# Performance work log

Measured on AMD Instinct MI355X. Metric: run time of the kernel, lower is better.

The kernel has to match this reference:

```python
import jax, jax.numpy as jnp
import numpy as np

B, T, D = 4, 256, 1024
E, DL, TOPK, H = 16, 64, 2, 4


def setup_inputs() -> dict:
    key = jax.random.key(0)
    ks = jax.random.split(key, 12)
    n = lambda k, s: (0.02 * jax.random.normal(k, s)).astype(jnp.float32)
    return dict(
        x=jax.random.normal(ks[0], (B, T, D), dtype=jnp.float32),
        w_down=n(ks[1], (E * DL, D)),
        pos_embed=n(ks[2], (1, E, DL)),
        gp_w=n(ks[3], (DL, D)), gp_b=jnp.zeros((DL,), jnp.float32),
        attn_in_w=n(ks[4], (3 * DL, DL)), attn_in_b=jnp.zeros((3 * DL,), jnp.float32),
        attn_out_w=n(ks[5], (DL, DL)), attn_out_b=jnp.zeros((DL,), jnp.float32),
        ln_w=jnp.ones((DL,), jnp.float32), ln_b=jnp.zeros((DL,), jnp.float32),
        ls_w=n(ks[6], (1, DL)), ls_b=jnp.zeros((1,), jnp.float32),
        g1_w=n(ks[7], (2 * DL, DL)), g1_b=jnp.zeros((2 * DL,), jnp.float32),
        g2_w=n(ks[8], (E, 2 * DL)), g2_b=jnp.zeros((E,), jnp.float32),
        w_up=n(ks[9], (E, DL, D)),
    )


def reference(x, w_down, pos_embed, gp_w, gp_b, attn_in_w, attn_in_b,
              attn_out_w, attn_out_b, ln_w, ln_b, ls_w, ls_b,
              g1_w, g1_b, g2_w, g2_b, w_up):
    Bq, Tq, Dm = x.shape
    N = Bq * Tq
    xf = x.reshape(N, Dm)
    # per-token per-expert low-rank features [N, E, DL]
    ef = (xf @ w_down.T).reshape(N, E, DL)
    # global context per batch element -> [B, DL]
    gctx = x.mean(axis=1) @ gp_w.T + gp_b
    gtok = jnp.repeat(gctx, Tq, axis=0)[:, None, :]  # [N, 1, DL]
    seq = jnp.concatenate([gtok, ef + pos_embed], axis=1)  # [N, E+1, DL]
    # tiny multihead self-attention over E+1 tokens, eval mode (no dropout)
    qkv = seq @ attn_in_w.T + attn_in_b
    q, k, v = jnp.split(qkv, 3, axis=-1)
    hd = DL // H
    sh = lambda t: t.reshape(N, E + 1, H, hd).transpose(0, 2, 1, 3)
    q, k, v = sh(q), sh(k), sh(v)
    scores = jnp.einsum('nhqd,nhkd->nhqk', q, k) / np.float32(np.sqrt(hd))
    attn = jax.nn.softmax(scores, axis=-1)
    ctx = jnp.einsum('nhqk,nhkd->nhqd', attn, v).transpose(0, 2, 1, 3).reshape(N, E + 1, DL)
    attn_out = ctx @ attn_out_w.T + attn_out_b
    h = attn_out + seq
    mu = h.mean(-1, keepdims=True)
    var = h.var(-1, keepdims=True)
    hn = (h - mu) / jnp.sqrt(var + 1e-5) * ln_w + ln_b
    refined = hn[:, 1:, :]  # drop global token -> [N, E, DL]
    local_logits = (refined @ ls_w.T + ls_b)[..., 0]  # [N, E]
    gb = jax.nn.gelu(gctx @ g1_w.T + g1_b, approximate=False) @ g2_w.T + g2_b  # [B, E]
    logits = local_logits + jnp.repeat(gb, Tq, axis=0)
    probs = jax.nn.softmax(logits, axis=-1)
    tw, ti = jax.lax.top_k(probs, TOPK)
    tw = tw / tw.sum(-1, keepdims=True)
    sel = jnp.take_along_axis(ef, ti[..., None], axis=1)  # [N, K, DL]
    act = jax.nn.gelu(sel, approximate=False)
    # gather per-token expert up-projections and batched vec-mat
    eo = jnp.einsum('nkd,nkdm->nkm', act, w_up[ti])  # [N, K, D]
    out = (eo * tw[..., None]).sum(axis=1).reshape(Bq, Tq, Dm)
    mean_prob = probs.mean(axis=0)
    one_hot = jnp.zeros_like(probs).at[jnp.arange(N)[:, None], ti].set(1.0)
    aux_loss = E * jnp.sum(mean_prob * one_hot.mean(axis=0))
    return out, aux_loss
```

## Files before the change

### kernel.cpp

```cpp
#include <hip/hip_runtime.h>
#include <math.h>

#define NB 4
#define TT 256
#define DMODEL 1024
#define NE 16
#define DLQ 64
#define NH 4
#define HD 16
#define SEQL 17
#define NTOK 1024

static constexpr size_t WS_EF    = 0;
static constexpr size_t WS_AH    = 1048576;
static constexpr size_t WS_AL    = 1572864;
static constexpr size_t WS_BH    = 2097152;
static constexpr size_t WS_BL    = 2621440;
static constexpr size_t WS_P1    = 3145728;
static constexpr size_t WS_ACT   = 4194304;
static constexpr size_t WS_AIWFH = 4259840;
static constexpr size_t WS_AIWFL = 4265984;
static constexpr size_t WS_AOWFH = 4272128;
static constexpr size_t WS_AOWFL = 4274176;
static constexpr size_t WS_PR    = 4308992;
static constexpr size_t WS_TI    = 4325376;
static constexpr size_t WS_GCTX  = 4326400;
static constexpr size_t WS_GB    = 4326656;

typedef __attribute__((ext_vector_type(8))) short short8;
typedef __attribute__((ext_vector_type(4))) float f32x4;

__device__ __forceinline__ float gelu_exact(float x) {
    return 0.5f * x * (1.0f + erff(x * 0.70710678118654752f));
}

__device__ __forceinline__ unsigned short f2bf(float f) {
    unsigned int u = __float_as_uint(f);
    unsigned int r = (u + 0x7fffu + ((u >> 16) & 1u)) >> 16;
    return (unsigned short)r;
}
__device__ __forceinline__ float bf2f(unsigned short h) {
    return __uint_as_float(((unsigned int)h) << 16);
}

#define DPP_ADD(v, ctrl) { int _m = __builtin_amdgcn_update_dpp(0, __float_as_int(v), ctrl, 0xF, 0xF, true); \
                           v += __int_as_float(_m); }
__device__ __forceinline__ float rsum16(float v) {
    DPP_ADD(v, 0x128);
    DPP_ADD(v, 0x124);
    DPP_ADD(v, 0x122);
    DPP_ADD(v, 0x121);
    return v;
}
__device__ __forceinline__ float rsum64(float v) {
    v = rsum16(v);
    v += __shfl_xor(v, 16);
    v += __shfl_xor(v, 32);
    return v;
}

__global__ __launch_bounds__(256) void k_prep(const float* __restrict__ x,
                                              const float* __restrict__ wdn,
                                              const float* __restrict__ aiw,
                                              const float* __restrict__ aow,
                                              const float* __restrict__ gp_w,
                                              const float* __restrict__ gp_b,
                                              const float* __restrict__ g1_w,
                                              const float* __restrict__ g1_b,
                                              const float* __restrict__ g2_w,
                                              const float* __restrict__ g2_b,
                                              float* __restrict__ ws) {
    __shared__ float xm[DMODEL];
    __shared__ float gc[DLQ];
    __shared__ float gb1[128];
    int bi = blockIdx.x;
    int tid = threadIdx.x;
    if (bi < 1024) {
        int which = bi >> 9;
        int t = (bi & 511) * 256 + tid;
        int row = t >> 7;
        int col0 = (t & 127) * 8;
        const float* src = which ? wdn : x;
        unsigned short* hp = (unsigned short*)(ws + (which ? WS_BH : WS_AH));
        unsigned short* lp = (unsigned short*)(ws + (which ? WS_BL : WS_AL));
        float4 v0 = *(const float4*)(src + (size_t)row * DMODEL + col0);
        float4 v1 = *(const float4*)(src + (size_t)row * DMODEL + col0 + 4);
        float vv[8] = {v0.x, v0.y, v0.z, v0.w, v1.x, v1.y, v1.z, v1.w};
        unsigned short h8[8], l8[8];
#pragma unroll
        for (int j = 0; j < 8; ++j) {
            h8[j] = f2bf(vv[j]);
            l8[j] = f2bf(vv[j] - bf2f(h8[j]));
        }
        int nb = row >> 6, kb = col0 >> 6;
        int st = (row & 63) >> 4;
        int ks = (col0 & 63) >> 5;
        int ln = (row & 15) + (((col0 >> 3) & 3) << 4);
        size_t off = (size_t)(nb * 16 + kb) * 4096 + st * 1024 + ks * 512 + ln * 8;
        *(short8*)(hp + off) = *(short8*)h8;
        *(short8*)(lp + off) = *(short8*)l8;
    } else if (bi < 1028) {
        int b = bi - 1024;
        int wv = tid >> 6, l = tid & 63;
        {
            const float* xb = x + (size_t)b * TT * DMODEL + tid * 4;
            float4 a = {0.f, 0.f, 0.f, 0.f};
#pragma unroll 4
            for (int t2 = 0; t2 < TT; ++t2) {
                float4 v = *(const float4*)(xb + (size_t)t2 * DMODEL);
                a.x += v.x; a.y += v.y; a.z += v.z; a.w += v.w;
            }
            const float inv_t = 1.0f / (float)TT;
            xm[tid * 4 + 0] = a.x * inv_t;
            xm[tid * 4 + 1] = a.y * inv_t;
            xm[tid * 4 + 2] = a.z * inv_t;
            xm[tid * 4 + 3] = a.w * inv_t;
        }
        __syncthreads();
        {
            const float* xp = xm + l * 16;
            float4 xv0 = *(const float4*)(xp);
            float4 xv1 = *(const float4*)(xp + 4);
            float4 xv2 = *(const float4*)(xp + 8);
            float4 xv3 = *(const float4*)(xp + 12);
            for (int rq = 0; rq < 4; ++rq) {
                int o = wv * 16 + rq * 4;
                float s[4];
#pragma unroll
                for (int r = 0; r < 4; ++r) {
                    const float* wr = gp_w + (size_t)(o + r) * DMODEL + l * 16;
                    float4 w0 = *(const float4*)(wr);
                    float4 w1 = *(const float4*)(wr + 4);
                    float4 w2 = *(const float4*)(wr + 8);
                    float4 w3 = *(const float4*)(wr + 12);
                    s[r] = w0.x * xv0.x + w0.y * xv0.y + w0.z * xv0.z + w0.w * xv0.w +
                           w1.x * xv1.x + w1.y * xv1.y + w1.z * xv1.z + w1.w * xv1.w +
                           w2.x * xv2.x + w2.y * xv2.y + w2.z * xv2.z + w2.w * xv2.w +
                           w3.x * xv3.x + w3.y * xv3.y + w3.z * xv3.z + w3.w * xv3.w;
                }
#pragma unroll
                for (int r = 0; r < 4; ++r) s[r] = rsum64(s[r]);
                if (l == 0) {
#pragma unroll
                    for (int r = 0; r < 4; ++r) {
                        float v = s[r] + gp_b[o + r];
                        gc[o + r] = v;
                        ws[WS_GCTX + b * DLQ + o + r] = v;
                    }
                }
            }
        }
        __syncthreads();
        {
            float gcl = gc[l];
            for (int rq = 0; rq < 8; ++rq) {
                int o = wv * 32 + rq * 4;
                float s[4];
#pragma unroll
                for (int r = 0; r < 4; ++r) s[r] = gcl * g1_w[(size_t)(o + r) * DLQ + l];
#pragma unroll
                for (int r = 0; r < 4; ++r) s[r] = rsum64(s[r]);
                if (l == 0) {
#pragma unroll
                    for (int r = 0; r < 4; ++r) gb1[o + r] = gelu_exact(s[r] + g1_b[o + r]);
                }
            }
        }
        __syncthreads();
        {
            float v0 = gb1[l * 2], v1 = gb1[l * 2 + 1];
            int o = wv * 4;
            float s[4];
#pragma unroll
            for (int r = 0; r < 4; ++r)
                s[r] = v0 * g2_w[(size_t)(o + r) * 128 + l * 2] +
                       v1 * g2_w[(size_t)(o + r) * 128 + l * 2 + 1];
#pragma unroll
            for (int r = 0; r < 4; ++r) s[r] = rsum64(s[r]);
            if (l == 0) {
#pragma unroll
                for (int r = 0; r < 4; ++r) ws[WS_GB + b * NE + o + r] = s[r] + g2_b[o + r];
            }
        }
    } else {
        unsigned short* fh = (unsigned short*)(ws + WS_AIWFH);
        unsigned short* fl = (unsigned short*)(ws + WS_AIWFL);
        for (int idx = tid; idx < 12 * 2 * 64; idx += 256) {
            int nt = idx >> 7, kf = (idx >> 6) & 1, l = idx & 63;
            int row = nt * 16 + (l & 15);
            int k = kf * 32 + ((l >> 4) << 3);
            const float* src = aiw + (size_t)row * DLQ + k;
            unsigned short h8[8], l8[8];
#pragma unroll
            for (int j = 0; j < 8; ++j) {
                h8[j] = f2bf(src[j]);
                l8[j] = f2bf(src[j] - bf2f(h8[j]));
            }
            size_t off = (size_t)(nt * 2 + kf) * 512 + l * 8;
            *(short8*)(fh + off) = *(short8*)h8;
            *(short8*)(fl + off) = *(short8*)l8;
        }
        unsigned short* gh = (unsigned short*)(ws + WS_AOWFH);
        unsigned short* gl = (unsigned short*)(ws + WS_AOWFL);
        for (int idx = tid; idx < 4 * 2 * 64; idx += 256) {
            int nt = idx >> 7, kf = (idx >> 6) & 1, l = idx & 63;
            int row = nt * 16 + (l & 15);
            int k = kf * 32 + ((l >> 4) << 3);
            const float* src = aow + (size_t)row * DLQ + k;
            unsigned short h8[8], l8[8];
#pragma unroll
            for (int j = 0; j < 8; ++j) {
                h8[j] = f2bf(src[j]);
                l8[j] = f2bf(src[j] - bf2f(h8[j]));
            }
            size_t off = (size_t)(nt * 2 + kf) * 512 + l * 8;
            *(short8*)(gh + off) = *(short8*)h8;
            *(short8*)(gl + off) = *(short8*)l8;
        }
    }
}

__global__ __launch_bounds__(256) void k_ef_mfma(float* __restrict__ ws) {
    __shared__ __attribute__((aligned(16))) unsigned short smem[16384];
    int tid = threadIdx.x;
    int bi = blockIdx.x;

    int xcd = bi & 7;
    int g   = bi >> 3;
    int kz  = g >> 5;
    int rem = g & 31;
    int nb  = (xcd >> 1) * 4 + (rem >> 3);
    int mb  = (xcd & 1) * 8 + (rem & 7);

    const unsigned short* AhP = (const unsigned short*)(ws + WS_AH);
    const unsigned short* AlP = (const unsigned short*)(ws + WS_AL);
    const unsigned short* BhP = (const unsigned short*)(ws + WS_BH);
    const unsigned short* BlP = (const unsigned short*)(ws + WS_BL);
    int w = tid >> 6, l = tid & 63;
    int wn = (w >> 1) * 32, wm = (w & 1) * 32;
    int stA = wn >> 4, stB = wm >> 4;
    f32x4 acc00 = {0.f, 0.f, 0.f, 0.f}, acc01 = acc00, acc10 = acc00, acc11 = acc00;

    for (int it = 0; it < 8; ++it) {
        int kb = kz * 8 + it;
        const char* srcs[4] = {
            (const char*)(AhP + (size_t)(nb * 16 + kb) * 4096),
            (const char*)(AlP + (size_t)(nb * 16 + kb) * 4096),
            (const char*)(BhP + (size_t)(mb * 16 + kb) * 4096),
            (const char*)(BlP + (size_t)(mb * 16 + kb) * 4096)};
#pragma unroll
        for (int p = 0; p < 4; ++p) {
#pragma unroll
            for (int h = 0; h < 2; ++h) {
                __builtin_amdgcn_global_load_lds(
                    (const __attribute__((address_space(1))) void*)(srcs[p] + h * 4096 + tid * 16),
                    (__attribute__((address_space(3))) void*)((char*)smem + p * 8192 + h * 4096 + tid * 16),
                    16, 0, 0);
            }
        }
        __syncthreads();
        const unsigned short* Ah = smem;
        const unsigned short* Al = smem + 4096;
        const unsigned short* Bh = smem + 8192;
        const unsigned short* Bl = smem + 12288;
#pragma unroll
        for (int ks = 0; ks < 2; ++ks) {
            short8 ah0 = *(const short8*)(Ah + (stA + 0) * 1024 + ks * 512 + l * 8);
            short8 ah1 = *(const short8*)(Ah + (stA + 1) * 1024 + ks * 512 + l * 8);
            short8 al0 = *(const short8*)(Al + (stA + 0) * 1024 + ks * 512 + l * 8);
            short8 al1 = *(const short8*)(Al + (stA + 1) * 1024 + ks * 512 + l * 8);
            short8 bh0 = *(const short8*)(Bh + (stB + 0) * 1024 + ks * 512 + l * 8);
            short8 bh1 = *(const short8*)(Bh + (stB + 1) * 1024 + ks * 512 + l * 8);
            short8 bl0 = *(const short8*)(Bl + (stB + 0) * 1024 + ks * 512 + l * 8);
            short8 bl1 = *(const short8*)(Bl + (stB + 1) * 1024 + ks * 512 + l * 8);
            acc00 = __builtin_amdgcn_mfma_f32_16x16x32_bf16(ah0, bh0, acc00, 0, 0, 0);
            acc00 = __builtin_amdgcn_mfma_f32_16x16x32_bf16(al0, bh0, acc00, 0, 0, 0);
            acc00 = __builtin_amdgcn_mfma_f32_16x16x32_bf16(ah0, bl0, acc00, 0, 0, 0);
            acc01 = __builtin_amdgcn_mfma_f32_16x16x32_bf16(ah0, bh1, acc01, 0, 0, 0);
            acc01 = __builtin_amdgcn_mfma_f32_16x16x32_bf16(al0, bh1, acc01, 0, 0, 0);
            acc01 = __builtin_amdgcn_mfma_f32_16x16x32_bf16(ah0, bl1, acc01, 0, 0, 0);
            acc10 = __builtin_amdgcn_mfma_f32_16x16x32_bf16(ah1, bh0, acc10, 0, 0, 0);
            acc10 = __builtin_amdgcn_mfma_f32_16x16x32_bf16(al1, bh0, acc10, 0, 0, 0);
            acc10 = __builtin_amdgcn_mfma_f32_16x16x32_bf16(ah1, bl0, acc10, 0, 0, 0);
            acc11 = __builtin_amdgcn_mfma_f32_16x16x32_bf16(ah1, bh1, acc11, 0, 0, 0);
            acc11 = __builtin_amdgcn_mfma_f32_16x16x32_bf16(al1, bh1, acc11, 0, 0, 0);
            acc11 = __builtin_amdgcn_mfma_f32_16x16x32_bf16(ah1, bl1, acc11, 0, 0, 0);
        }
        __syncthreads();
    }
    int cr = (l >> 4) * 4, cc = l & 15;
    int n0 = nb * 64, m0 = mb * 64;
    float* P = ws + (kz == 0 ? WS_EF : WS_P1);
#pragma unroll
    for (int r = 0; r < 4; ++r) {
        P[(size_t)(n0 + wn + cr + r) * DMODEL + (m0 + wm + cc)]           = acc00[r];
        P[(size_t)(n0 + wn + cr + r) * DMODEL + (m0 + wm + 16 + cc)]      = acc01[r];
        P[(size_t)(n0 + wn + 16 + cr + r) * DMODEL + (m0 + wm + cc)]      = acc10[r];
        P[(size_t)(n0 + wn + 16 + cr + r) * DMODEL + (m0 + wm + 16 + cc)] = acc11[r];
    }
}

__global__ __launch_bounds__(128) void k_attn2(const float* __restrict__ pos_embed,
                                               const float* __restrict__ attn_in_b,
                                               const float* __restrict__ attn_out_b,
                                               const float* __restrict__ ln_w,
                                               const float* __restrict__ ln_b,
                                               const float* __restrict__ ls_w,
                                               const float* __restrict__ ls_b,
                                               float* __restrict__ ws) {
    int n = blockIdx.x;
    int w = threadIdx.x >> 6;
    int l = threadIdx.x & 63;
    int b = n >> 8;

    __shared__ float qkv[SEQL * 200];
    __shared__ __attribute__((aligned(16))) char ubuf[8192];
    __shared__ __attribute__((aligned(16))) unsigned short ctxH[1024];
    __shared__ __attribute__((aligned(16))) unsigned short ctxL[1024];
    __shared__ float lgv_sh[NE];
    unsigned short* sH = (unsigned short*)ubuf;
    unsigned short* sL = (unsigned short*)(ubuf + 4096);
    float* ao = (float*)ubuf;

    float seqc[SEQL];
    {
        const float* efp0 = ws + WS_EF + (size_t)n * DMODEL;
        const float* efp1 = ws + WS_P1 + (size_t)n * DMODEL;
        float gcv = ws[WS_GCTX + b * DLQ + l];
#pragma unroll
        for (int i = 0; i < SEQL; ++i) {
            float s = (i == 0) ? gcv
                               : efp0[(i - 1) * DLQ + l] + efp1[(i - 1) * DLQ + l] +
                                 pos_embed[(i - 1) * DLQ + l];
            seqc[i] = s;
            int lo_r = w * 9, hi_r = w * 9 + 8;
            if (i >= lo_r && i <= hi_r && i < SEQL) {
                unsigned short hs = f2bf(s);
                unsigned short lsv = f2bf(s - bf2f(hs));
                int mt = i >> 4;
                int ls = (i & 15) + (((l >> 3) & 3) << 4);
                int kf = l >> 5;
                int j = l & 7;
                size_t off = (size_t)(mt * 2 + kf) * 512 + ls * 8 + j;
                sH[off] = hs;
                sL[off] = lsv;
            }
        }
    }
    __syncthreads();

    {
        const unsigned short* fh = (const unsigned short*)(ws + WS_AIWFH);
        const unsigned short* fl = (const unsigned short*)(ws + WS_AIWFL);
        f32x4 acc[6][2];
#pragma unroll
        for (int t = 0; t < 6; ++t)
#pragma unroll
            for (int m = 0; m < 2; ++m) acc[t][m] = (f32x4){0.f, 0.f, 0.f, 0.f};
#pragma unroll
        for (int kf = 0; kf < 2; ++kf) {
            short8 ah0 = *(const short8*)(sH + (0 * 2 + kf) * 512 + l * 8);
            short8 ah1 = *(const short8*)(sH + (1 * 2 + kf) * 512 + l * 8);
            short8 al0 = *(const short8*)(sL + (0 * 2 + kf) * 512 + l * 8);
            short8 al1 = *(const short8*)(sL + (1 * 2 + kf) * 512 + l * 8);
#pragma unroll
            for (int t = 0; t < 6; ++t) {
                int nt = w * 6 + t;
                short8 bh = *(const short8*)(fh + (size_t)(nt * 2 + kf) * 512 + l * 8);
                short8 bl = *(const short8*)(fl + (size_t)(nt * 2 + kf) * 512 + l * 8);
                acc[t][0] = __builtin_amdgcn_mfma_f32_16x16x32_bf16(ah0, bh, acc[t][0], 0, 0, 0);
                acc[t][0] = __builtin_amdgcn_mfma_f32_16x16x32_bf16(al0, bh, acc[t][0], 0, 0, 0);
                acc[t][0] = __builtin_amdgcn_mfma_f32_16x16x32_bf16(ah0, bl, acc[t][0], 0, 0, 0);
                acc[t][1] = __builtin_amdgcn_mfma_f32_16x16x32_bf16(ah1, bh, acc[t][1], 0, 0, 0);
                acc[t][1] = __builtin_amdgcn_mfma_f32_16x16x32_bf16(al1, bh, acc[t][1], 0, 0, 0);
                acc[t][1] = __builtin_amdgcn_mfma_f32_16x16x32_bf16(ah1, bl, acc[t][1], 0, 0, 0);
            }
        }
#pragma unroll
        for (int t = 0; t < 6; ++t) {
            int col = (w * 6 + t) * 16 + (l & 15);
            float bias = attn_in_b[col];
#pragma unroll
            for (int r = 0; r < 4; ++r) {
                int row = (l >> 4) * 4 + r;
                qkv[row * 200 + col] = acc[t][0][r] + bias;
            }
            if ((l >> 4) == 0) qkv[16 * 200 + col] = acc[t][1][0] + bias;
        }
    }
    __syncthreads();

    {
        int g = l >> 4;
        float kc[SEQL], vc[SEQL];
#pragma unroll
        for (int j = 0; j < SEQL; ++j) {
            kc[j] = qkv[j * 200 + 64 + g * 16 + (l & 15)];
            vc[j] = qkv[j * 200 + 128 + l];
        }
        for (int i = w * 8 + 1; i <= w * 8 + 8; ++i) {
            float qi = qkv[i * 200 + g * 16 + (l & 15)];
            float sj[SEQL];
#pragma unroll
            for (int j = 0; j < SEQL; ++j) {
                sj[j] = rsum16(qi * kc[j]) * 0.25f;
            }
            float m = sj[0];
#pragma unroll
            for (int j = 1; j < SEQL; ++j) m = fmaxf(m, sj[j]);
            float ssum = 0.f;
#pragma unroll
            for (int j = 0; j < SEQL; ++j) { sj[j] = __expf(sj[j] - m); ssum += sj[j]; }
            float inv = 1.f / ssum;
            float c = 0.f;
#pragma unroll
            for (int j = 0; j < SEQL; ++j) c += sj[j] * vc[j];
            c *= inv;
            unsigned short ch = f2bf(c);
            unsigned short cl = f2bf(c - bf2f(ch));
            int ls = ((i - 1) & 15) + (((l >> 3) & 3) << 4);
            int kf = l >> 5;
            int j2 = l & 7;
            size_t off = (size_t)kf * 512 + ls * 8 + j2;
            ctxH[off] = ch;
            ctxL[off] = cl;
        }
    }
    __syncthreads();

    {
        const unsigned short* gh = (const unsigned short*)(ws + WS_AOWFH);
        const unsigned short* gl = (const unsigned short*)(ws + WS_AOWFL);
        f32x4 acc[2];
        acc[0] = (f32x4){0.f, 0.f, 0.f, 0.f};
        acc[1] = acc[0];
#pragma unroll
        for (int kf = 0; kf < 2; ++kf) {
            short8 ah = *(const short8*)(ctxH + kf * 512 + l * 8);
            short8 al = *(const short8*)(ctxL + kf * 512 + l * 8);
#pragma unroll
            for (int t = 0; t < 2; ++t) {
                int nt = w * 2 + t;
                short8 bh = *(const short8*)(gh + (size_t)(nt * 2 + kf) * 512 + l * 8);
                short8 bl = *(const short8*)(gl + (size_t)(nt * 2 + kf) * 512 + l * 8);
                acc[t] = __builtin_amdgcn_mfma_f32_16x16x32_bf16(ah, bh, acc[t], 0, 0, 0);
                acc[t] = __builtin_amdgcn_mfma_f32_16x16x32_bf16(al, bh, acc[t], 0, 0, 0);
                acc[t] = __builtin_amdgcn_mfma_f32_16x16x32_bf16(ah, bl, acc[t], 0, 0, 0);
            }
        }
        __syncthreads();
#pragma unroll
        for (int t = 0; t < 2; ++t) {
            int col = (w * 2 + t) * 16 + (l & 15);
            float bias = attn_out_b[col];
#pragma unroll
            for (int r = 0; r < 4; ++r) {
                int row = (l >> 4) * 4 + r;
                ao[row * 72 + col] = acc[t][r] + bias;
            }
        }
    }
    __syncthreads();

    float rs[SEQL];
#pragma unroll
    for (int i = 1; i < SEQL; ++i) rs[i] = seqc[i] + ao[(i - 1) * 72 + l];

    float c1 = ln_w[l] * ls_w[l];
    float c1sum = rsum64(c1);
    float c0sum = rsum64(ln_b[l] * ls_w[l]);
    float lsb0 = ls_b[0];
#pragma unroll
    for (int ee = 0; ee < 8; ++ee) {
        int e = w * 8 + ee;
        float x = rs[e + 1];
        float s1 = rsum64(x);
        float s2 = rsum64(x * x);
        float s3 = rsum64(x * c1);
        float mu = s1 * (1.0f / DLQ);
        float var = s2 * (1.0f / DLQ) - mu * mu;
        float rstd = rsqrtf(var + 1e-5f);
        float lgv = rstd * (s3 - mu * c1sum) + c0sum + lsb0 + ws[WS_GB + b * NE + e];
        if (l == 0) lgv_sh[e] = lgv;
    }
    __syncthreads();

    if (w == 0) {
        float p[NE];
        float lgv[NE];
#pragma unroll
        for (int e = 0; e < NE; ++e) lgv[e] = lgv_sh[e];
        float m = lgv[0];
#pragma unroll
        for (int e = 1; e < NE; ++e) m = fmaxf(m, lgv[e]);
        float ssum = 0.f;
#pragma unroll
        for (int e = 0; e < NE; ++e) { p[e] = __expf(lgv[e] - m); ssum += p[e]; }
        float inv = 1.f / ssum;
#pragma unroll
        for (int e = 0; e < NE; ++e) p[e] *= inv;
        int t0 = 0; float b0 = p[0];
#pragma unroll
        for (int e = 1; e < NE; ++e) if (p[e] > b0) { b0 = p[e]; t0 = e; }
        int t1 = -1; float b1 = -1.f;
#pragma unroll
        for (int e = 0; e < NE; ++e) if (e != t0 && p[e] > b1) { b1 = p[e]; t1 = e; }

        float sw = b0 + b1;
        float tw0 = b0 / sw, tw1 = b1 / sw;
        unsigned short* actp = (unsigned short*)(ws + WS_ACT);
        float efv0 = ws[WS_EF + (size_t)n * DMODEL + t0 * DLQ + l] +
                     ws[WS_P1 + (size_t)n * DMODEL + t0 * DLQ + l];
        float efv1 = ws[WS_EF + (size_t)n * DMODEL + t1 * DLQ + l] +
                     ws[WS_P1 + (size_t)n * DMODEL + t1 * DLQ + l];
        actp[(size_t)(n * 2 + 0) * 64 + l] = f2bf(gelu_exact(efv0) * tw0);
        actp[(size_t)(n * 2 + 1) * 64 + l] = f2bf(gelu_exact(efv1) * tw1);
        if (l == 0) {
#pragma unroll
            for (int e = 0; e < NE; ++e) ws[WS_PR + (size_t)n * NE + e] = p[e];
            ((int*)(ws + WS_TI))[n] = t0 | (t1 << 8);
        }
    }
}

__global__ __launch_bounds__(256) void k_moe_gemm(const float* __restrict__ w_up,
                                                  float* __restrict__ ws,
                                                  float* __restrict__ out) {
    __shared__ int lst[2048];
    __shared__ int lcnt;
    __shared__ float wsum[4][NE];
    __shared__ int hist[NE];
    int tid = threadIdx.x;
    int wv = tid >> 6, l = tid & 63;

    if (blockIdx.x == NE) {
        if (blockIdx.y != 0) return;
        if (tid < NE) hist[tid] = 0;
        __syncthreads();
        {
            const int* tip = (const int*)(ws + WS_TI);
#pragma unroll
            for (int c = 0; c < 4; ++c) {
                int pk = tip[tid * 4 + c];
                atomicAdd(&hist[pk & 0xff], 1);
                atomicAdd(&hist[(pk >> 8) & 0xff], 1);
            }
        }
        float p[NE];
#pragma unroll
        for (int e = 0; e < NE; ++e) p[e] = 0.f;
        const float* pr = ws + WS_PR + (size_t)tid * 64;
#pragma unroll
        for (int r = 0; r < 4; ++r)
#pragma unroll
            for (int q = 0; q < 4; ++q) {
                float4 v = *(const float4*)(pr + r * 16 + q * 4);
                p[q * 4 + 0] += v.x; p[q * 4 + 1] += v.y;
                p[q * 4 + 2] += v.z; p[q * 4 + 3] += v.w;
            }
#pragma unroll
        for (int e = 0; e < NE; ++e) p[e] = rsum64(p[e]);
        if (l == 0) {
#pragma unroll
            for (int e = 0; e < NE; ++e) wsum[wv][e] = p[e];
        }
        __syncthreads();
        if (tid == 0) {
            float s = 0.f;
#pragma unroll
            for (int e = 0; e < NE; ++e) {
                float sp = wsum[0][e] + wsum[1][e] + wsum[2][e] + wsum[3][e];
                s += sp * (float)hist[e];
            }
            out[(size_t)NTOK * DMODEL] = (float)NE * s / ((float)NTOK * (float)NTOK);
        }
        return;
    }

    int e = blockIdx.x, ct = blockIdx.y;
    if (tid == 0) lcnt = 0;
    __syncthreads();
    {
        const int* tip = (const int*)(ws + WS_TI);
#pragma unroll
        for (int c = 0; c < 4; ++c) {
            int tok = wv * 256 + c * 64 + l;
            int pk = tip[tok];
            bool m1 = ((pk >> 8) & 0xff) == e;
            bool m = ((pk & 0xff) == e) || m1;
            unsigned long long mask = __ballot(m);
            int base = 0;
            if (l == 0 && mask) base = atomicAdd(&lcnt, __popcll(mask));
            base = __shfl(base, 0);
            if (m) {
                int pos = base + __popcll(mask & ((1ull << l) - 1ull));
                lst[pos] = tok * 2 + (m1 ? 1 : 0);
            }
        }
    }
    __syncthreads();
    int cnt = lcnt;
    if (cnt == 0) return;

    int col = ct * 64 + wv * 16 + (l & 15);
    int kb = (l >> 4) * 8;
    const float* wue = w_up + (size_t)e * DLQ * DMODEL + col;
    unsigned short b0v[8], b1v[8];
#pragma unroll
    for (int j = 0; j < 8; ++j) {
        b0v[j] = f2bf(wue[(size_t)(kb + j) * DMODEL]);
        b1v[j] = f2bf(wue[(size_t)(kb + 32 + j) * DMODEL]);
    }
    short8 bf0 = *(short8*)b0v;
    short8 bf1 = *(short8*)b1v;

    const unsigned short* actp = (const unsigned short*)(ws + WS_ACT);
    int cr = (l >> 4) * 4;

    for (int mt = 0; mt < cnt; mt += 16) {
        int row = mt + (l & 15);
        short8 a0 = {0, 0, 0, 0, 0, 0, 0, 0};
        short8 a1 = {0, 0, 0, 0, 0, 0, 0, 0};
        if (row < cnt) {
            int pk = lst[row];
            a0 = *(const short8*)(actp + (size_t)pk * 64 + kb);
            a1 = *(const short8*)(actp + (size_t)pk * 64 + 32 + kb);
        }
        f32x4 acc = {0.f, 0.f, 0.f, 0.f};
        acc = __builtin_amdgcn_mfma_f32_16x16x32_bf16(a0, bf0, acc, 0, 0, 0);
        acc = __builtin_amdgcn_mfma_f32_16x16x32_bf16(a1, bf1, acc, 0, 0, 0);
#pragma unroll
        for (int r = 0; r < 4; ++r) {
            int rr = mt + cr + r;
            if (rr < cnt) {
                int pk = lst[rr];
                atomicAdd(&out[(size_t)(pk >> 1) * DMODEL + col], acc[r]);
            }
        }
    }
}

extern "C" void kernel_launch(void* const* d_in, const int* in_sizes, int n_in,
                              void* d_out, int out_size, void* d_ws, size_t ws_size,
                              hipStream_t stream) {
    const float* x          = (const float*)d_in[0];
    const float* w_down     = (const float*)d_in[1];
    const float* pos_embed  = (const float*)d_in[2];
    const float* gp_w       = (const float*)d_in[3];
    const float* gp_b       = (const float*)d_in[4];
    const float* attn_in_w  = (const float*)d_in[5];
    const float* attn_in_b  = (const float*)d_in[6];
    const float* attn_out_w = (const float*)d_in[7];
    const float* attn_out_b = (const float*)d_in[8];
    const float* ln_w       = (const float*)d_in[9];
    const float* ln_b       = (const float*)d_in[10];
    const float* ls_w       = (const float*)d_in[11];
    const float* ls_b       = (const float*)d_in[12];
    const float* g1_w       = (const float*)d_in[13];
    const float* g1_b       = (const float*)d_in[14];
    const float* g2_w       = (const float*)d_in[15];
    const float* g2_b       = (const float*)d_in[16];
    const float* w_up       = (const float*)d_in[17];
    float* ws  = (float*)d_ws;
    float* out = (float*)d_out;

    hipMemsetAsync(out, 0, (size_t)out_size * sizeof(float), stream);
    k_prep<<<1029, 256, 0, stream>>>(x, w_down, attn_in_w, attn_out_w,
                                     gp_w, gp_b, g1_w, g1_b, g2_w, g2_b, ws);
    k_ef_mfma<<<512, 256, 0, stream>>>(ws);
    k_attn2<<<NTOK, 128, 0, stream>>>(pos_embed, attn_in_b, attn_out_b,
                                      ln_w, ln_b, ls_w, ls_b, ws);
    k_moe_gemm<<<dim3(NE + 1, 16), 256, 0, stream>>>(w_up, ws, out);
}
```

Measured before the change: 184.8 us.

## Compute global context via per-token gp_w projection in the MFMA GEMM

The old k_prep block sequentially reduced x over 256 tokens per batch on only four blocks, which was a long serial tail. Now gp_w is split into bf16 hi/lo and appended as extra tiles in the ef MFMA GEMM (x@gp_w^T per token), and a small new kernel averages the per-token projections and runs the g1/g2 MLP. This uses the linearity of the mean to move the reduction after the projection, at the cost of an extra kernel launch and extra GEMM and workspace traffic.

After: 165.9 us. 10.2% less time.

```diff
diff --git a/kernel.cpp b/kernel.cpp
--- a/kernel.cpp
+++ b/kernel.cpp
@@ -26,6 +26,10 @@
 static constexpr size_t WS_TI    = 4325376;
 static constexpr size_t WS_GCTX  = 4326400;
 static constexpr size_t WS_GB    = 4326656;
+static constexpr size_t WS_GPH   = 4400128;
+static constexpr size_t WS_GPL   = 4432896;
+static constexpr size_t WS_GPX0  = 4465664;
+static constexpr size_t WS_GPX1  = 4531200;
 
 typedef __attribute__((ext_vector_type(8))) short short8;
 typedef __attribute__((ext_vector_type(4))) float f32x4;
@@ -61,18 +65,10 @@
 
 __global__ __launch_bounds__(256) void k_prep(const float* __restrict__ x,
                                               const float* __restrict__ wdn,
+                                              const float* __restrict__ gp_w,
                                               const float* __restrict__ aiw,
                                               const float* __restrict__ aow,
-                                              const float* __restrict__ gp_w,
-                                              const float* __restrict__ gp_b,
-                                              const float* __restrict__ g1_w,
-                                              const float* __restrict__ g1_b,
-                                              const float* __restrict__ g2_w,
-                                              const float* __restrict__ g2_b,
                                               float* __restrict__ ws) {
-    __shared__ float xm[DMODEL];
-    __shared__ float gc[DLQ];
-    __shared__ float gb1[128];
     int bi = blockIdx.x;
     int tid = threadIdx.x;
     if (bi < 1024) {
@@ -99,89 +95,28 @@
         size_t off = (size_t)(nb * 16 + kb) * 4096 + st * 1024 + ks * 512 + ln * 8;
         *(short8*)(hp + off) = *(short8*)h8;
         *(short8*)(lp + off) = *(short8*)l8;
-    } else if (bi < 1028) {
-        int b = bi - 1024;
-        int wv = tid >> 6, l = tid & 63;
-        {
-            const float* xb = x + (size_t)b * TT * DMODEL + tid * 4;
-            float4 a = {0.f, 0.f, 0.f, 0.f};
-#pragma unroll 4
-            for (int t2 = 0; t2 < TT; ++t2) {
-                float4 v = *(const float4*)(xb + (size_t)t2 * DMODEL);
-                a.x += v.x; a.y += v.y; a.z += v.z; a.w += v.w;
-            }
-            const float inv_t = 1.0f / (float)TT;
-            xm[tid * 4 + 0] = a.x * inv_t;
-            xm[tid * 4 + 1] = a.y * inv_t;
-            xm[tid * 4 + 2] = a.z * inv_t;
-            xm[tid * 4 + 3] = a.w * inv_t;
-        }
-        __syncthreads();
-        {
-            const float* xp = xm + l * 16;
-            float4 xv0 = *(const float4*)(xp);
-            float4 xv1 = *(const float4*)(xp + 4);
-            float4 xv2 = *(const float4*)(xp + 8);
-            float4 xv3 = *(const float4*)(xp + 12);
-            for (int rq = 0; rq < 4; ++rq) {
-                int o = wv * 16 + rq * 4;
-                float s[4];
-#pragma unroll
-                for (int r = 0; r < 4; ++r) {
-                    const float* wr = gp_w + (size_t)(o + r) * DMODEL + l * 16;
-                    float4 w0 = *(const float4*)(wr);
-                    float4 w1 = *(const float4*)(wr + 4);
-                    float4 w2 = *(const float4*)(wr + 8);
-                    float4 w3 = *(const float4*)(wr + 12);
-                    s[r] = w0.x * xv0.x + w0.y * xv0.y + w0.z * xv0.z + w0.w * xv0.w +
-                           w1.x * xv1.x + w1.y * xv1.y + w1.z * xv1.z + w1.w * xv1.w +
-                           w2.x * xv2.x + w2.y * xv2.y + w2.z * xv2.z + w2.w * xv2.w +
-                           w3.x * xv3.x + w3.y * xv3.y + w3.z * xv3.z + w3.w * xv3.w;
-                }
-#pragma unroll
-                for (int r = 0; r < 4; ++r) s[r] = rsum64(s[r]);
-                if (l == 0) {
-#pragma unroll
-                    for (int r = 0; r < 4; ++r) {
-                        float v = s[r] + gp_b[o + r];
-                        gc[o + r] = v;
-                        ws[WS_GCTX + b * DLQ + o + r] = v;
-                    }
-                }
-            }
-        }
-        __syncthreads();
-        {
-            float gcl = gc[l];
-            for (int rq = 0; rq < 8; ++rq) {
-                int o = wv * 32 + rq * 4;
-                float s[4];
-#pragma unroll
-                for (int r = 0; r < 4; ++r) s[r] = gcl * g1_w[(size_t)(o + r) * DLQ + l];
-#pragma unroll
-                for (int r = 0; r < 4; ++r) s[r] = rsum64(s[r]);
-                if (l == 0) {
-#pragma unroll
-                    for (int r = 0; r < 4; ++r) gb1[o + r] = gelu_exact(s[r] + g1_b[o + r]);
-                }
-            }
-        }
-        __syncthreads();
-        {
-            float v0 = gb1[l * 2], v1 = gb1[l * 2 + 1];
-            int o = wv * 4;
-            float s[4];
-#pragma unroll
-            for (int r = 0; r < 4; ++r)
-                s[r] = v0 * g2_w[(size_t)(o + r) * 128 + l * 2] +
-                       v1 * g2_w[(size_t)(o + r) * 128 + l * 2 + 1];
-#pragma unroll
-            for (int r = 0; r < 4; ++r) s[r] = rsum64(s[r]);
-            if (l == 0) {
-#pragma unroll
-                for (int r = 0; r < 4; ++r) ws[WS_GB + b * NE + o + r] = s[r] + g2_b[o + r];
-            }
-        }
+    } else if (bi < 1056) {
+        int t = (bi - 1024) * 256 + tid;
+        int row = t >> 7;
+        int col0 = (t & 127) * 8;
+        unsigned short* hp = (unsigned short*)(ws + WS_GPH);
+        unsigned short* lp = (unsigned short*)(ws + WS_GPL);
+        float4 v0 = *(const float4*)(gp_w + (size_t)row * DMODEL + col0);
+        float4 v1 = *(const float4*)(gp_w + (size_t)row * DMODEL + col0 + 4);
+        float vv[8] = {v0.x, v0.y, v0.z, v0.w, v1.x, v1.y, v1.z, v1.w};
+        unsigned short h8[8], l8[8];
+#pragma unroll
+        for (int j = 0; j < 8; ++j) {
+            h8[j] = f2bf(vv[j]);
+            l8[j] = f2bf(vv[j] - bf2f(h8[j]));
+        }
+        int kb = col0 >> 6;
+        int st = row >> 4;
+        int ks = (col0 & 63) >> 5;
+        int ln = (row & 15) + (((col0 >> 3) & 3) << 4);
+        size_t off = (size_t)kb * 4096 + st * 1024 + ks * 512 + ln * 8;
+        *(short8*)(hp + off) = *(short8*)h8;
+        *(short8*)(lp + off) = *(short8*)l8;
     } else {
         unsigned short* fh = (unsigned short*)(ws + WS_AIWFH);
         unsigned short* fl = (unsigned short*)(ws + WS_AIWFL);
@@ -225,17 +160,28 @@
     int tid = threadIdx.x;
     int bi = blockIdx.x;
 
-    int xcd = bi & 7;
-    int g   = bi >> 3;
-    int kz  = g >> 5;
-    int rem = g & 31;
-    int nb  = (xcd >> 1) * 4 + (rem >> 3);
-    int mb  = (xcd & 1) * 8 + (rem & 7);
+    int nb, mb, kz;
+    bool gp = bi >= 512;
+    if (gp) {
+        int idx = bi - 512;
+        nb = idx & 15;
+        kz = idx >> 4;
+        mb = 0;
+    } else {
+        int xcd = bi & 7;
+        int g   = bi >> 3;
+        kz  = g >> 5;
+        int rem = g & 31;
+        nb  = (xcd >> 1) * 4 + (rem >> 3);
+        mb  = (xcd & 1) * 8 + (rem & 7);
+    }
 
     const unsigned short* AhP = (const unsigned short*)(ws + WS_AH);
     const unsigned short* AlP = (const unsigned short*)(ws + WS_AL);
-    const unsigned short* BhP = (const unsigned short*)(ws + WS_BH);
-    const unsigned short* BlP = (const unsigned short*)(ws + WS_BL);
+    const unsigned short* BhP = gp ? (const unsigned short*)(ws + WS_GPH)
+                                   : (const unsigned short*)(ws + WS_BH);
+    const unsigned short* BlP = gp ? (const unsigned short*)(ws + WS_GPL)
+                                   : (const unsigned short*)(ws + WS_BL);
     int w = tid >> 6, l = tid & 63;
     int wn = (w >> 1) * 32, wm = (w & 1) * 32;
     int stA = wn >> 4, stB = wm >> 4;
@@ -289,14 +235,85 @@
         __syncthreads();
     }
     int cr = (l >> 4) * 4, cc = l & 15;
-    int n0 = nb * 64, m0 = mb * 64;
-    float* P = ws + (kz == 0 ? WS_EF : WS_P1);
+    int n0 = nb * 64;
+    float* P;
+    size_t rstride;
+    int m0;
+    if (gp) {
+        P = ws + (kz == 0 ? WS_GPX0 : WS_GPX1);
+        rstride = 64;
+        m0 = 0;
+    } else {
+        P = ws + (kz == 0 ? WS_EF : WS_P1);
+        rstride = DMODEL;
+        m0 = mb * 64;
+    }
 #pragma unroll
     for (int r = 0; r < 4; ++r) {
-        P[(size_t)(n0 + wn + cr + r) * DMODEL + (m0 + wm + cc)]           = acc00[r];
-        P[(size_t)(n0 + wn + cr + r) * DMODEL + (m0 + wm + 16 + cc)]      = acc01[r];
-        P[(size_t)(n0 + wn + 16 + cr + r) * DMODEL + (m0 + wm + cc)]      = acc10[r];
-        P[(size_t)(n0 + wn + 16 + cr + r) * DMODEL + (m0 + wm + 16 + cc)] = acc11[r];
+        P[(size_t)(n0 + wn + cr + r) * rstride + (m0 + wm + cc)]           = acc00[r];
+        P[(size_t)(n0 + wn + cr + r) * rstride + (m0 + wm + 16 + cc)]      = acc01[r];
+        P[(size_t)(n0 + wn + 16 + cr + r) * rstride + (m0 + wm + cc)]      = acc10[r];
+        P[(size_t)(n0 + wn + 16 + cr + r) * rstride + (m0 + wm + 16 + cc)] = acc11[r];
+    }
+}
+
+__global__ __launch_bounds__(256) void k_gctx(const float* __restrict__ gp_b,
+                                              const float* __restrict__ g1_w,
+                                              const float* __restrict__ g1_b,
+                                              const float* __restrict__ g2_w,
+                                              const float* __restrict__ g2_b,
+                                              float* __restrict__ ws) {
+    __shared__ float part[4][DLQ];
+    __shared__ float gc[DLQ];
+    __shared__ float gb1[128];
+    int b = blockIdx.x;
+    int tid = threadIdx.x;
+    int wv = tid >> 6, l = tid & 63;
+    {
+        const float* g0 = ws + WS_GPX0 + (size_t)(b * 256 + wv * 64) * 64 + l;
+        const float* g1p = ws + WS_GPX1 + (size_t)(b * 256 + wv * 64) * 64 + l;
+        float s = 0.f;
+#pragma unroll 8
+        for (int t = 0; t < 64; ++t) s += g0[t * 64] + g1p[t * 64];
+        part[wv][l] = s;
+    }
+    __syncthreads();
+    if (wv == 0) {
+        float v = (part[0][l] + part[1][l] + part[2][l] + part[3][l]) * (1.0f / TT) + gp_b[l];
+        gc[l] = v;
+        ws[WS_GCTX + b * DLQ + l] = v;
+    }
+    __syncthreads();
+    {
+        float gcl = gc[l];
+        for (int rq = 0; rq < 8; ++rq) {
+            int o = wv * 32 + rq * 4;
+            float s[4];
+#pragma unroll
+            for (int r = 0; r < 4; ++r) s[r] = gcl * g1_w[(size_t)(o + r) * DLQ + l];
+#pragma unroll
+            for (int r = 0; r < 4; ++r) s[r] = rsum64(s[r]);
+            if (l == 0) {
+#pragma unroll
+                for (int r = 0; r < 4; ++r) gb1[o + r] = gelu_exact(s[r] + g1_b[o + r]);
+            }
+        }
+    }
+    __syncthreads();
+    {
+        float v0 = gb1[l * 2], v1 = gb1[l * 2 + 1];
+        int o = wv * 4;
+        float s[4];
+#pragma unroll
+        for (int r = 0; r < 4; ++r)
+            s[r] = v0 * g2_w[(size_t)(o + r) * 128 + l * 2] +
+                   v1 * g2_w[(size_t)(o + r) * 128 + l * 2 + 1];
+#pragma unroll
+        for (int r = 0; r < 4; ++r) s[r] = rsum64(s[r]);
+        if (l == 0) {
+#pragma unroll
+            for (int r = 0; r < 4; ++r) ws[WS_GB + b * NE + o + r] = s[r] + g2_b[o + r];
+        }
     }
 }
 
@@ -665,9 +682,9 @@
     float* out = (float*)d_out;
 
     hipMemsetAsync(out, 0, (size_t)out_size * sizeof(float), stream);
-    k_prep<<<1029, 256, 0, stream>>>(x, w_down, attn_in_w, attn_out_w,
-                                     gp_w, gp_b, g1_w, g1_b, g2_w, g2_b, ws);
-    k_ef_mfma<<<512, 256, 0, stream>>>(ws);
+    k_prep<<<1057, 256, 0, stream>>>(x, w_down, gp_w, attn_in_w, attn_out_w, ws);
+    k_ef_mfma<<<544, 256, 0, stream>>>(ws);
+    k_gctx<<<NB, 256, 0, stream>>>(gp_b, g1_w, g1_b, g2_w, g2_b, ws);
     k_attn2<<<NTOK, 128, 0, stream>>>(pos_embed, attn_in_b, attn_out_b,
                                       ln_w, ln_b, ls_w, ls_b, ws);
     k_moe_gemm<<<dim3(NE + 1, 16), 256, 0, stream>>>(w_up, ws, out);
```
